# Optimization experiments

Measured on AMD Instinct MI355X. Metric: run time of the kernel, lower is better.

The kernel has to match this reference:

```python
import jax, jax.numpy as jnp
import numpy as np

N = 50000      # nodes
F_IN = 1024    # raw feature dim
D = 64         # student_dim = hidden_dim * compression_ratio
P = 3          # number of meta-paths
E = 1600000    # edges per meta-path adjacency (avg degree 32)


def setup_inputs() -> dict:
    key = jax.random.key(0)
    ks = jax.random.split(key, 10)
    feats = jax.random.normal(ks[0], (N, F_IN), jnp.float32)
    rows = jax.random.randint(ks[1], (P, E), 0, N, dtype=jnp.int32)
    cols = jax.random.randint(ks[2], (P, E), 0, N, dtype=jnp.int32)
    # normalized-adjacency-like positive edge weights
    vals = jax.random.uniform(ks[3], (P, E), jnp.float32) / 32.0
    # fc_list[0]: Linear(F_IN -> D), xavier_normal gain=1.414
    W0 = jax.random.normal(ks[4], (D, F_IN), jnp.float32) * 0.05
    b0 = jnp.zeros((D,), jnp.float32)
    # P GCN linear layers (D -> D, no bias) + GCN bias params
    Wg = jax.random.normal(ks[5], (P, D, D), jnp.float32) * 0.17
    bg = jnp.zeros((P, D), jnp.float32)
    # PReLU alpha (torch default init 0.25, one scalar per GCN)
    alpha = jnp.full((P,), 0.25, jnp.float32)
    # Attention: Linear(D -> D) and att vector [1, D]
    Wa = jax.random.normal(ks[6], (D, D), jnp.float32) * 0.17
    ba = jnp.zeros((D,), jnp.float32)
    att = jax.random.normal(ks[7], (1, D), jnp.float32) * 0.17
    return dict(feats=feats, rows=rows, cols=cols, vals=vals, W0=W0, b0=b0,
                Wg=Wg, bg=bg, alpha=alpha, Wa=Wa, ba=ba, att=att)


def reference(feats, rows, cols, vals, W0, b0, Wg, bg, alpha, Wa, ba, att):
    # h = elu(fc_list[0](feats))  (feat_drop = 0 -> identity)
    h = jax.nn.elu(feats @ W0.T + b0)                       # [N, D]
    embeds = []
    for i in range(P):
        s = h @ Wg[i].T                                     # [N, D]
        # sparse adj (COO) @ s : out[r] += v * s[c]
        msg = vals[i][:, None] * s[cols[i]]                 # [E, D]
        out = jax.ops.segment_sum(msg, rows[i], num_segments=N)
        out = out + bg[i]
        embeds.append(jnp.where(out > 0, out, alpha[i] * out))  # PReLU
    emb = jnp.stack(embeds)                                 # [P, N, D]
    # Attention over views: beta_i = att . mean_n tanh(fc(emb_i))
    sp = jnp.tanh(jnp.einsum('pnd,ed->pne', emb, Wa) + ba).mean(axis=1)  # [P, D]
    beta = jax.nn.softmax(sp @ att[0])                      # [P]
    z_mp = jnp.einsum('p,pnd->nd', beta, emb)               # [N, D]
    return z_mp
```

## Files before the change

kernel.cpp:

```cpp
#include <hip/hip_runtime.h>
#include <hip/hip_bf16.h>

#define N_NODES 50000
#define F_IN    1024
#define DD      64
#define PP      3
#define EE      1600000
#define NPC     98
#define CCAP    17664

typedef __attribute__((ext_vector_type(8))) short short8v;
typedef __attribute__((ext_vector_type(4))) float floatx4;
typedef __attribute__((ext_vector_type(2))) float floatx2;

__device__ inline float bfl(uint u) { return __uint_as_float(u << 16); }
__device__ inline float bfh(uint u) { return __uint_as_float(u & 0xffff0000u); }
__device__ inline floatx2 up2(uint u) {
    floatx2 r; r.x = bfl(u); r.y = bfh(u); return r;
}
__device__ inline uint cvtpk2(float a, float b) {
    __hip_bfloat162 h = __float22bfloat162_rn(make_float2(a, b));
    return *(uint*)&h;
}
__device__ inline ushort f2bf(float x) {
    __hip_bfloat16 h = __float2bfloat16(x);
    return *(ushort*)&h;
}

__global__ __launch_bounds__(256) void split_weights(const float* __restrict__ W0,
                                                     const float* __restrict__ Wg,
                                                     const float* __restrict__ Wa,
                                                     ushort* __restrict__ W0h,
                                                     ushort* __restrict__ Wgh,
                                                     ushort* __restrict__ Wah)
{
    int i = blockIdx.x * 256 + threadIdx.x;
    if (i < 64 * 1024) W0h[i] = f2bf(W0[i]);
    int j = i - 64 * 1024;
    if (j >= 0 && j < PP * 64 * 64) Wgh[j] = f2bf(Wg[j]);
    int k = i - 64 * 1024 - PP * 64 * 64;
    if (k >= 0 && k < 64 * 64) Wah[k] = f2bf(Wa[k]);
}

__global__ __launch_bounds__(256) void gemm1_partial(const float* __restrict__ feats,
                                                     const ushort* __restrict__ W0h,
                                                     float* __restrict__ hpart)
{
    __shared__ ushort Ah[64 * 64];
    __shared__ ushort Bh[64 * 64];
    const int t = threadIdx.x;
    const int w = t >> 6, lane = t & 63;
    const int row0 = blockIdx.x * 64;
    const int kh = blockIdx.y;
    const int l15 = lane & 15, l4 = lane >> 4;

    floatx4 acc[4] = {};
    float4 pa[4];
    uint4  pb[2];

    #pragma unroll
    for (int rep = 0; rep < 4; ++rep) {
        int idx = rep * 256 + t;
        int r = idx >> 4, c4 = idx & 15;
        int gr = row0 + r; if (gr >= N_NODES) gr = N_NODES - 1;
        pa[rep] = *(const float4*)&feats[(size_t)gr * F_IN + (kh * 8) * 64 + c4 * 4];
    }
    #pragma unroll
    for (int rep = 0; rep < 2; ++rep) {
        int idx = rep * 256 + t;
        int c = idx >> 3, u8 = idx & 7;
        pb[rep] = *(const uint4*)&W0h[(size_t)c * F_IN + (kh * 8) * 64 + u8 * 8];
    }

    for (int kc = 0; kc < 8; ++kc) {
        #pragma unroll
        for (int rep = 0; rep < 4; ++rep) {
            int idx = rep * 256 + t;
            int r = idx >> 4, c4 = idx & 15;
            int unit = (c4 >> 1) ^ (r & 7);
            int base = r * 64 + unit * 8 + (c4 & 1) * 4;
            *(uint2*)&Ah[base] = make_uint2(cvtpk2(pa[rep].x, pa[rep].y),
                                            cvtpk2(pa[rep].z, pa[rep].w));
        }
        #pragma unroll
        for (int rep = 0; rep < 2; ++rep) {
            int idx = rep * 256 + t;
            int c = idx >> 3, u8 = idx & 7;
            int unit = u8 ^ (c & 7);
            *(uint4*)&Bh[c * 64 + unit * 8] = pb[rep];
        }
        __syncthreads();

        if (kc < 7) {
            int g = kh * 8 + kc + 1;
            #pragma unroll
            for (int rep = 0; rep < 4; ++rep) {
                int idx = rep * 256 + t;
                int r = idx >> 4, c4 = idx & 15;
                int gr = row0 + r; if (gr >= N_NODES) gr = N_NODES - 1;
                pa[rep] = *(const float4*)&feats[(size_t)gr * F_IN + g * 64 + c4 * 4];
            }
            #pragma unroll
            for (int rep = 0; rep < 2; ++rep) {
                int idx = rep * 256 + t;
                int c = idx >> 3, u8 = idx & 7;
                pb[rep] = *(const uint4*)&W0h[(size_t)c * F_IN + g * 64 + u8 * 8];
            }
        }

        #pragma unroll
        for (int ks = 0; ks < 2; ++ks) {
            int arow = w * 16 + l15;
            int au = (ks * 4 + l4) ^ (arow & 7);
            short8v ah = *(short8v*)&Ah[arow * 64 + au * 8];
            #pragma unroll
            for (int cf = 0; cf < 4; ++cf) {
                int bcol = cf * 16 + l15;
                int bu = (ks * 4 + l4) ^ (bcol & 7);
                short8v bh = *(short8v*)&Bh[bcol * 64 + bu * 8];
                acc[cf] = __builtin_amdgcn_mfma_f32_16x16x32_bf16(ah, bh, acc[cf], 0, 0, 0);
            }
        }
        __syncthreads();
    }

    float* hp = hpart + ((size_t)(kh * 782 + blockIdx.x)) * 4096;
    #pragma unroll
    for (int cf = 0; cf < 4; ++cf)
        *(float4*)&hp[(cf * 256 + t) * 4] = make_float4(acc[cf][0], acc[cf][1],
                                                        acc[cf][2], acc[cf][3]);
}

__global__ __launch_bounds__(256) void gemm2_combine(const float* __restrict__ hpart,
                                                     const float* __restrict__ b0,
                                                     const ushort* __restrict__ Wgh,
                                                     ushort* __restrict__ s_all)
{
    __shared__ ushort Ah[64 * 64];
    __shared__ ushort Bh[64 * 64];
    __shared__ ushort Sout[64 * 64];
    const int t = threadIdx.x;
    const int w = t >> 6, lane = t & 63;
    const int row0 = blockIdx.x * 64;
    const int l15 = lane & 15, l4 = lane >> 4;

    const float* hp0 = hpart + (size_t)blockIdx.x * 4096;
    const float* hp1 = hpart + (size_t)(782 + blockIdx.x) * 4096;

    #pragma unroll
    for (int cf = 0; cf < 4; ++cf) {
        float4 a = *(const float4*)&hp0[(cf * 256 + t) * 4];
        float4 b = *(const float4*)&hp1[(cf * 256 + t) * 4];
        int col = cf * 16 + l15;
        float bias = b0[col];
        float xs[4] = {a.x + b.x + bias, a.y + b.y + bias,
                       a.z + b.z + bias, a.w + b.w + bias};
        #pragma unroll
        for (int r = 0; r < 4; ++r) {
            int row = w * 16 + l4 * 4 + r;
            float x = xs[r];
            x = x > 0.f ? x : (__expf(x) - 1.f);
            int u = (col >> 3) ^ (row & 7);
            Ah[row * 64 + u * 8 + (col & 7)] = f2bf(x);
        }
    }
    __syncthreads();

    for (int p = 0; p < PP; ++p) {
        #pragma unroll
        for (int rep = 0; rep < 2; ++rep) {
            int idx = rep * 256 + t;
            int r = idx >> 3, u8 = idx & 7;
            int unit = u8 ^ (r & 7);
            *(uint4*)&Bh[r * 64 + unit * 8] = *(const uint4*)&Wgh[(size_t)p * 4096 + idx * 8];
        }
        __syncthreads();

        floatx4 sacc[4] = {};
        #pragma unroll
        for (int ks = 0; ks < 2; ++ks) {
            int arow = w * 16 + l15;
            int au = (ks * 4 + l4) ^ (arow & 7);
            short8v ah = *(short8v*)&Ah[arow * 64 + au * 8];
            #pragma unroll
            for (int cf = 0; cf < 4; ++cf) {
                int bcol = cf * 16 + l15;
                int bu = (ks * 4 + l4) ^ (bcol & 7);
                short8v bh = *(short8v*)&Bh[bcol * 64 + bu * 8];
                sacc[cf] = __builtin_amdgcn_mfma_f32_16x16x32_bf16(ah, bh, sacc[cf], 0, 0, 0);
            }
        }
        #pragma unroll
        for (int cf = 0; cf < 4; ++cf) {
            int col = cf * 16 + l15;
            #pragma unroll
            for (int r = 0; r < 4; ++r)
                Sout[(w * 16 + l4 * 4 + r) * 64 + col] = f2bf(sacc[cf][r]);
        }
        __syncthreads();
        {
            int lr = t >> 2;
            int gr = row0 + lr;
            if (gr < N_NODES) {
                ushort* sp = s_all + (size_t)p * N_NODES * 64;
                int co = (t & 3) * 16;
                *(uint4*)&sp[(size_t)gr * 64 + co]     = *(uint4*)&Sout[lr * 64 + co];
                *(uint4*)&sp[(size_t)gr * 64 + co + 8] = *(uint4*)&Sout[lr * 64 + co + 8];
            }
        }
        __syncthreads();
    }
}

__global__ __launch_bounds__(256) void part1(const int*   __restrict__ rows,
                                             const int*   __restrict__ cols,
                                             const float* __restrict__ vals,
                                             int*   __restrict__ pcur3,
                                             uint2* __restrict__ coarsebuf)
{
    __shared__ uint2 stage[2560];
    __shared__ uint2 sorted[2560];
    __shared__ int cnt[128];
    __shared__ int sc[128];
    __shared__ int curb[128];
    __shared__ int gbase[128];
    const int t = threadIdx.x;
    const int path = blockIdx.y;
    const size_t ebase = (size_t)path * EE + (size_t)blockIdx.x * 2560;
    int* pcur = pcur3 + path * NPC;
    uint2* cb = coarsebuf + (size_t)path * NPC * CCAP;

    if (t < 128) { cnt[t] = 0; curb[t] = 0; }
    __syncthreads();

    #pragma unroll
    for (int it = 0; it < 10; ++it) {
        int e = it * 256 + t;
        int r = rows[ebase + e];
        int c = cols[ebase + e];
        float v = vals[ebase + e];
        int bin = r >> 9, rl = r & 511;
        stage[e] = make_uint2((uint)c | ((uint)rl << 16) | ((uint)bin << 25),
                              __float_as_uint(v));
        atomicAdd(&cnt[bin], 1);
    }
    __syncthreads();

    if (t < 128) sc[t] = cnt[t];
    __syncthreads();
    #pragma unroll
    for (int o = 1; o < 128; o <<= 1) {
        int v = (t < 128 && t >= o) ? sc[t - o] : 0;
        __syncthreads();
        if (t < 128 && t >= o) sc[t] += v;
        __syncthreads();
    }

    if (t < NPC) gbase[t] = atomicAdd(&pcur[t], cnt[t]);
    __syncthreads();

    #pragma unroll
    for (int it = 0; it < 10; ++it) {
        uint2 e = stage[it * 256 + t];
        int bin = e.x >> 25;
        int loc = (sc[bin] - cnt[bin]) + atomicAdd(&curb[bin], 1);
        sorted[loc] = e;
    }
    __syncthreads();

    #pragma unroll
    for (int it = 0; it < 10; ++it) {
        int i = it * 256 + t;
        uint2 e = sorted[i];
        int bin = e.x >> 25;
        int g = gbase[bin] + (i - (sc[bin] - cnt[bin]));
        if (g < CCAP) cb[(size_t)bin * CCAP + g] = e;
    }
}

__global__ __launch_bounds__(512) void sort2(const uint2* __restrict__ coarsebuf,
                                             const int*   __restrict__ pcur3,
                                             uint* __restrict__ sortpk,
                                             int* __restrict__ rowbeg3,
                                             int* __restrict__ rowend3)
{
    __shared__ int hist[512];
    __shared__ int cur[512];
    const int t = threadIdx.x;
    const int c = blockIdx.x, path = blockIdx.y;
    const int n = min(pcur3[path * NPC + c], CCAP);
    const size_t slabbase = ((size_t)path * NPC + c) * CCAP;
    const uint2* src = coarsebuf + slabbase;

    hist[t] = 0;
    __syncthreads();

    for (int i = t; i < n; i += 512)
        atomicAdd(&hist[(src[i].x >> 16) & 511], 1);
    __syncthreads();

    int c0 = hist[t];
    __syncthreads();
    #pragma unroll
    for (int o = 1; o < 512; o <<= 1) {
        int v = (t >= o) ? hist[t - o] : 0;
        __syncthreads();
        hist[t] += v;
        __syncthreads();
    }
    int excl = hist[t] - c0;
    cur[t] = excl;
    int gr = c * 512 + t;
    if (gr < N_NODES) {
        rowbeg3[path * N_NODES + gr] = (int)(slabbase + excl);
        rowend3[path * N_NODES + gr] = (int)(slabbase + excl + c0);
    }
    __syncthreads();

    for (int i = t; i < n; i += 512) {
        uint2 e = src[i];
        int rl = (e.x >> 16) & 511;
        int pos = atomicAdd(&cur[rl], 1);
        sortpk[slabbase + pos] = (e.x & 0xffffu) |
                                 ((uint)f2bf(__uint_as_float(e.y)) << 16);
    }
}

__global__ __launch_bounds__(256) void spmm_gather(const uint*   __restrict__ sortpk,
                                                   const int*    __restrict__ rowbeg3,
                                                   const int*    __restrict__ rowend3,
                                                   const ushort* __restrict__ s_all,
                                                   const float*  __restrict__ bg,
                                                   const float*  __restrict__ alpha,
                                                   ushort* __restrict__ emb)
{
    const int path = blockIdx.x / 12500;
    const int wid = (blockIdx.x % 12500) * 4 + (threadIdx.x >> 6);
    const int lane = threadIdx.x & 63;
    const int dq = lane & 7;
    const int slot = lane >> 3;
    const int e0 = rowbeg3[path * N_NODES + wid];
    const int e1 = rowend3[path * N_NODES + wid];
    const ushort* s_p = s_all + (size_t)path * N_NODES * 64;

    floatx2 acc[4] = {};
    if (e0 < e1) {
        const int last = e1 - 1;
        for (int e = e0; e < e1; e += 32) {
            int ea = e + slot, eb = ea + 8, ec = ea + 16, ed = ea + 24;
            uint pka = sortpk[min(ea, last)];
            uint pkb = sortpk[min(eb, last)];
            uint pkc = sortpk[min(ec, last)];
            uint pkd = sortpk[min(ed, last)];
            const uint4 ga = *(const uint4*)&s_p[(size_t)(pka & 0xffffu) * 64 + dq * 8];
            const uint4 gb = *(const uint4*)&s_p[(size_t)(pkb & 0xffffu) * 64 + dq * 8];
            const uint4 gc = *(const uint4*)&s_p[(size_t)(pkc & 0xffffu) * 64 + dq * 8];
            const uint4 gd = *(const uint4*)&s_p[(size_t)(pkd & 0xffffu) * 64 + dq * 8];
            float va = (ea <= last) ? bfh(pka) : 0.f;
            float vb = (eb <= last) ? bfh(pkb) : 0.f;
            float vc = (ec <= last) ? bfh(pkc) : 0.f;
            float vd = (ed <= last) ? bfh(pkd) : 0.f;
            floatx2 va2 = {va, va}, vb2 = {vb, vb}, vc2 = {vc, vc}, vd2 = {vd, vd};
            acc[0] += va2 * up2(ga.x); acc[1] += va2 * up2(ga.y);
            acc[2] += va2 * up2(ga.z); acc[3] += va2 * up2(ga.w);
            acc[0] += vb2 * up2(gb.x); acc[1] += vb2 * up2(gb.y);
            acc[2] += vb2 * up2(gb.z); acc[3] += vb2 * up2(gb.w);
            acc[0] += vc2 * up2(gc.x); acc[1] += vc2 * up2(gc.y);
            acc[2] += vc2 * up2(gc.z); acc[3] += vc2 * up2(gc.w);
            acc[0] += vd2 * up2(gd.x); acc[1] += vd2 * up2(gd.y);
            acc[2] += vd2 * up2(gd.z); acc[3] += vd2 * up2(gd.w);
        }
    }
    #pragma unroll
    for (int j = 0; j < 4; ++j) {
        acc[j].x += __shfl_xor(acc[j].x, 8);
        acc[j].y += __shfl_xor(acc[j].y, 8);
        acc[j].x += __shfl_xor(acc[j].x, 16);
        acc[j].y += __shfl_xor(acc[j].y, 16);
        acc[j].x += __shfl_xor(acc[j].x, 32);
        acc[j].y += __shfl_xor(acc[j].y, 32);
    }

    if (slot == 0) {
        const float al = alpha[path];
        const float* bgp = bg + path * 64;
        float x[8];
        #pragma unroll
        for (int j = 0; j < 4; ++j) {
            float v0 = acc[j].x + bgp[dq * 8 + 2 * j];
            float v1 = acc[j].y + bgp[dq * 8 + 2 * j + 1];
            x[2 * j]     = v0 > 0.f ? v0 : al * v0;
            x[2 * j + 1] = v1 > 0.f ? v1 : al * v1;
        }
        uint4 wv;
        wv.x = cvtpk2(x[0], x[1]);
        wv.y = cvtpk2(x[2], x[3]);
        wv.z = cvtpk2(x[4], x[5]);
        wv.w = cvtpk2(x[6], x[7]);
        *(uint4*)&emb[((size_t)path * N_NODES + wid) * 64 + dq * 8] = wv;
    }
}

__global__ __launch_bounds__(256) void postproc(const ushort* __restrict__ emb,
                                                const ushort* __restrict__ Wah,
                                                const float* __restrict__ ba,
                                                float* __restrict__ sp)
{
    __shared__ ushort Ah[64 * 64];
    __shared__ ushort Bh[64 * 64];
    __shared__ float red[16][64];
    const int t = threadIdx.x;
    const int w = t >> 6, lane = t & 63;
    const int l15 = lane & 15, l4 = lane >> 4;
    const int nb = (N_NODES + 63) >> 6;
    const int p  = blockIdx.x / nb;
    const int tb = blockIdx.x % nb;
    const int row0 = tb * 64;
    const ushort* embp = emb + (size_t)p * N_NODES * 64;

    #pragma unroll
    for (int rep = 0; rep < 2; ++rep) {
        int idx = rep * 256 + t;
        int r = idx >> 3, u8 = idx & 7;
        int gr = row0 + r; if (gr >= N_NODES) gr = N_NODES - 1;
        int unit = u8 ^ (r & 7);
        *(uint4*)&Ah[r * 64 + unit * 8] = *(const uint4*)&embp[(size_t)gr * 64 + u8 * 8];
        *(uint4*)&Bh[r * 64 + unit * 8] = *(const uint4*)&Wah[idx * 8];
    }
    __syncthreads();

    floatx4 acc[4] = {};
    #pragma unroll
    for (int ks = 0; ks < 2; ++ks) {
        int arow = w * 16 + l15;
        int au = (ks * 4 + l4) ^ (arow & 7);
        short8v ah = *(short8v*)&Ah[arow * 64 + au * 8];
        #pragma unroll
        for (int cf = 0; cf < 4; ++cf) {
            int bcol = cf * 16 + l15;
            int bu = (ks * 4 + l4) ^ (bcol & 7);
            short8v bh = *(short8v*)&Bh[bcol * 64 + bu * 8];
            acc[cf] = __builtin_amdgcn_mfma_f32_16x16x32_bf16(ah, bh, acc[cf], 0, 0, 0);
        }
    }

    #pragma unroll
    for (int cf = 0; cf < 4; ++cf) {
        int col = cf * 16 + l15;
        float s = 0.f;
        #pragma unroll
        for (int r = 0; r < 4; ++r) {
            int gr = row0 + w * 16 + l4 * 4 + r;
            if (gr < N_NODES) s += tanhf(acc[cf][r] + ba[col]);
        }
        red[w * 4 + l4][col] = s;
    }
    __syncthreads();
    if (t < 64) {
        float ssum = 0.f;
        #pragma unroll
        for (int g = 0; g < 16; ++g) ssum += red[g][t];
        unsafeAtomicAdd(&sp[p * 64 + t], ssum);
    }
}

__global__ void beta_kernel(const float* __restrict__ sp,
                            const float* __restrict__ att,
                            float* __restrict__ beta)
{
    int lane = threadIdx.x;
    float w[PP];
    #pragma unroll
    for (int p = 0; p < PP; ++p) {
        float x = sp[p * 64 + lane] * (1.0f / (float)N_NODES) * att[lane];
        #pragma unroll
        for (int off = 32; off; off >>= 1) x += __shfl_down(x, off);
        w[p] = __shfl(x, 0);
    }
    if (lane == 0) {
        float mx = fmaxf(w[0], fmaxf(w[1], w[2]));
        float e0 = __expf(w[0] - mx);
        float e1 = __expf(w[1] - mx);
        float e2 = __expf(w[2] - mx);
        float s = e0 + e1 + e2;
        beta[0] = e0 / s; beta[1] = e1 / s; beta[2] = e2 / s;
    }
}

__global__ __launch_bounds__(256) void combine(const ushort* __restrict__ emb,
                                               const float* __restrict__ beta,
                                               float* __restrict__ out)
{
    const float b0 = beta[0], b1 = beta[1], b2 = beta[2];
    const size_t tot = (size_t)N_NODES * 64;
    size_t i = ((size_t)blockIdx.x * 256 + threadIdx.x) * 8;
    if (i < tot) {
        uint4 e0 = *(const uint4*)&emb[i];
        uint4 e1 = *(const uint4*)&emb[tot + i];
        uint4 e2 = *(const uint4*)&emb[2 * tot + i];
        float o[8];
        o[0] = b0*bfl(e0.x) + b1*bfl(e1.x) + b2*bfl(e2.x);
        o[1] = b0*bfh(e0.x) + b1*bfh(e1.x) + b2*bfh(e2.x);
        o[2] = b0*bfl(e0.y) + b1*bfl(e1.y) + b2*bfl(e2.y);
        o[3] = b0*bfh(e0.y) + b1*bfh(e1.y) + b2*bfh(e2.y);
        o[4] = b0*bfl(e0.z) + b1*bfl(e1.z) + b2*bfl(e2.z);
        o[5] = b0*bfh(e0.z) + b1*bfh(e1.z) + b2*bfh(e2.z);
        o[6] = b0*bfl(e0.w) + b1*bfl(e1.w) + b2*bfl(e2.w);
        o[7] = b0*bfh(e0.w) + b1*bfh(e1.w) + b2*bfh(e2.w);
        *(float4*)&out[i]     = make_float4(o[0], o[1], o[2], o[3]);
        *(float4*)&out[i + 4] = make_float4(o[4], o[5], o[6], o[7]);
    }
}

extern "C" void kernel_launch(void* const* d_in, const int* in_sizes, int n_in,
                              void* d_out, int out_size, void* d_ws, size_t ws_size,
                              hipStream_t stream)
{
    const float* feats = (const float*)d_in[0];
    const int*   rows  = (const int*)  d_in[1];
    const int*   cols  = (const int*)  d_in[2];
    const float* vals  = (const float*)d_in[3];
    const float* W0    = (const float*)d_in[4];
    const float* b0    = (const float*)d_in[5];
    const float* Wg    = (const float*)d_in[6];
    const float* bg    = (const float*)d_in[7];
    const float* alpha = (const float*)d_in[8];
    const float* Wa    = (const float*)d_in[9];
    const float* ba    = (const float*)d_in[10];
    const float* att   = (const float*)d_in[11];
    float* out = (float*)d_out;

    const size_t ND = (size_t)N_NODES * 64;
    char* base = (char*)d_ws;
    ushort* emb    = (ushort*)base;              base += 3 * ND * 2;
    ushort* s_all  = (ushort*)base;              base += 3 * ND * 2;
    ushort* W0h    = (ushort*)base;              base += 64 * 1024 * 2;
    ushort* Wgh    = (ushort*)base;              base += PP * 64 * 64 * 2;
    ushort* Wah    = (ushort*)base;              base += 64 * 64 * 2;
    int*    pcur3  = (int*)base;                 base += PP * NPC * 4;
    float*  sp     = (float*)base;               base += 192 * 4;
    float*  beta   = (float*)base;               base += 64 * 4;
    int*    rowbeg3 = (int*)base;                base += PP * N_NODES * 4;
    int*    rowend3 = (int*)base;                base += PP * N_NODES * 4;
    base = (char*)(((size_t)base + 255) & ~(size_t)255);
    float*  hpart  = (float*)base;               base += (size_t)2 * 782 * 4096 * 4;
    uint2*  coarsebuf = (uint2*)base;            base += (size_t)PP * NPC * CCAP * 8;
    uint*   sortpk    = (uint*)base;             base += (size_t)PP * NPC * CCAP * 4;

    hipMemsetAsync(pcur3, 0, (PP * NPC + 192) * sizeof(int), stream);

    split_weights<<<(64 * 1024 + PP * 64 * 64 + 64 * 64 + 255) / 256, 256, 0, stream>>>(
        W0, Wg, Wa, W0h, Wgh, Wah);

    gemm1_partial<<<dim3(782, 2), 256, 0, stream>>>(feats, W0h, hpart);
    gemm2_combine<<<782, 256, 0, stream>>>(hpart, b0, Wgh, s_all);

    part1<<<dim3(EE / 2560, 3), 256, 0, stream>>>(rows, cols, vals, pcur3, coarsebuf);
    sort2<<<dim3(NPC, 3), 512, 0, stream>>>(coarsebuf, pcur3, sortpk, rowbeg3, rowend3);
    spmm_gather<<<3 * 12500, 256, 0, stream>>>(
        sortpk, rowbeg3, rowend3, s_all, bg, alpha, emb);

    postproc<<<3 * 782, 256, 0, stream>>>(emb, Wah, ba, sp);
    beta_kernel<<<1, 64, 0, stream>>>(sp, att, beta);
    combine<<<(int)((ND / 8 + 255) / 256), 256, 0, stream>>>(emb, beta, out);
}
```

Measured before the change: 319.4 us.

## Stage full W0 half-slice in LDS and stream feats directly into MFMA registers

gemm1_partial now uses 512-thread blocks covering 128 rows. Each block loads its whole 64x512 bf16 slice of W0 into LDS once. Each lane then reads its feats A-fragments straight from global memory, converts them to bf16 in registers and feeds the MFMA, so A no longer goes through LDS and the per-chunk barriers are gone. This is meant to remove the LDS staging and sync overhead of the memory-bound first GEMM. The trade-off is 64KB of LDS per block, which limits occupancy, and direct global loads of feats with no explicit prefetch. gemm2_combine's indexing into hpart is updated to match the new partial layout.

```diff
diff --git a/kernel.cpp b/kernel.cpp
--- a/kernel.cpp
+++ b/kernel.cpp
@@ -8,6 +8,7 @@
 #define EE      1600000
 #define NPC     98
 #define CCAP    17664
+#define NB1     391
 
 typedef __attribute__((ext_vector_type(8))) short short8v;
 typedef __attribute__((ext_vector_type(4))) float floatx4;
@@ -42,92 +43,52 @@
     if (k >= 0 && k < 64 * 64) Wah[k] = f2bf(Wa[k]);
 }
 
-__global__ __launch_bounds__(256) void gemm1_partial(const float* __restrict__ feats,
+__global__ __launch_bounds__(512) void gemm1_partial(const float* __restrict__ feats,
                                                      const ushort* __restrict__ W0h,
                                                      float* __restrict__ hpart)
 {
-    __shared__ ushort Ah[64 * 64];
-    __shared__ ushort Bh[64 * 64];
+    __shared__ ushort Bh[64 * 512];
     const int t = threadIdx.x;
     const int w = t >> 6, lane = t & 63;
-    const int row0 = blockIdx.x * 64;
+    const int row0 = blockIdx.x * 128;
     const int kh = blockIdx.y;
     const int l15 = lane & 15, l4 = lane >> 4;
 
+    #pragma unroll
+    for (int rep = 0; rep < 8; ++rep) {
+        int id = rep * 512 + t;
+        int d = id >> 6, uu = id & 63;
+        *(uint4*)&Bh[d * 512 + ((uu ^ (d & 7)) << 3)] =
+            *(const uint4*)&W0h[(size_t)d * F_IN + kh * 512 + uu * 8];
+    }
+    __syncthreads();
+
+    int gr = row0 + w * 16 + l15;
+    if (gr >= N_NODES) gr = N_NODES - 1;
+    const float* arow = feats + (size_t)gr * F_IN + kh * 512 + l4 * 8;
+
     floatx4 acc[4] = {};
-    float4 pa[4];
-    uint4  pb[2];
-
-    #pragma unroll
-    for (int rep = 0; rep < 4; ++rep) {
-        int idx = rep * 256 + t;
-        int r = idx >> 4, c4 = idx & 15;
-        int gr = row0 + r; if (gr >= N_NODES) gr = N_NODES - 1;
-        pa[rep] = *(const float4*)&feats[(size_t)gr * F_IN + (kh * 8) * 64 + c4 * 4];
-    }
-    #pragma unroll
-    for (int rep = 0; rep < 2; ++rep) {
-        int idx = rep * 256 + t;
-        int c = idx >> 3, u8 = idx & 7;
-        pb[rep] = *(const uint4*)&W0h[(size_t)c * F_IN + (kh * 8) * 64 + u8 * 8];
-    }
-
-    for (int kc = 0; kc < 8; ++kc) {
-        #pragma unroll
-        for (int rep = 0; rep < 4; ++rep) {
-            int idx = rep * 256 + t;
-            int r = idx >> 4, c4 = idx & 15;
-            int unit = (c4 >> 1) ^ (r & 7);
-            int base = r * 64 + unit * 8 + (c4 & 1) * 4;
-            *(uint2*)&Ah[base] = make_uint2(cvtpk2(pa[rep].x, pa[rep].y),
-                                            cvtpk2(pa[rep].z, pa[rep].w));
-        }
-        #pragma unroll
-        for (int rep = 0; rep < 2; ++rep) {
-            int idx = rep * 256 + t;
-            int c = idx >> 3, u8 = idx & 7;
-            int unit = u8 ^ (c & 7);
-            *(uint4*)&Bh[c * 64 + unit * 8] = pb[rep];
-        }
-        __syncthreads();
-
-        if (kc < 7) {
-            int g = kh * 8 + kc + 1;
-            #pragma unroll
-            for (int rep = 0; rep < 4; ++rep) {
-                int idx = rep * 256 + t;
-                int r = idx >> 4, c4 = idx & 15;
-                int gr = row0 + r; if (gr >= N_NODES) gr = N_NODES - 1;
-                pa[rep] = *(const float4*)&feats[(size_t)gr * F_IN + g * 64 + c4 * 4];
-            }
-            #pragma unroll
-            for (int rep = 0; rep < 2; ++rep) {
-                int idx = rep * 256 + t;
-                int c = idx >> 3, u8 = idx & 7;
-                pb[rep] = *(const uint4*)&W0h[(size_t)c * F_IN + g * 64 + u8 * 8];
-            }
-        }
-
-        #pragma unroll
-        for (int ks = 0; ks < 2; ++ks) {
-            int arow = w * 16 + l15;
-            int au = (ks * 4 + l4) ^ (arow & 7);
-            short8v ah = *(short8v*)&Ah[arow * 64 + au * 8];
-            #pragma unroll
-            for (int cf = 0; cf < 4; ++cf) {
-                int bcol = cf * 16 + l15;
-                int bu = (ks * 4 + l4) ^ (bcol & 7);
-                short8v bh = *(short8v*)&Bh[bcol * 64 + bu * 8];
-                acc[cf] = __builtin_amdgcn_mfma_f32_16x16x32_bf16(ah, bh, acc[cf], 0, 0, 0);
-            }
-        }
-        __syncthreads();
-    }
-
-    float* hp = hpart + ((size_t)(kh * 782 + blockIdx.x)) * 4096;
+    #pragma unroll 4
+    for (int ks = 0; ks < 16; ++ks) {
+        float4 a0 = *(const float4*)&arow[ks * 32];
+        float4 a1 = *(const float4*)&arow[ks * 32 + 4];
+        uint4 av;
+        av.x = cvtpk2(a0.x, a0.y); av.y = cvtpk2(a0.z, a0.w);
+        av.z = cvtpk2(a1.x, a1.y); av.w = cvtpk2(a1.z, a1.w);
+        short8v ah = *(short8v*)&av;
+        int u = ks * 4 + l4;
+        #pragma unroll
+        for (int cf = 0; cf < 4; ++cf) {
+            int d = cf * 16 + l15;
+            short8v bh = *(short8v*)&Bh[d * 512 + ((u ^ (d & 7)) << 3)];
+            acc[cf] = __builtin_amdgcn_mfma_f32_16x16x32_bf16(ah, bh, acc[cf], 0, 0, 0);
+        }
+    }
+
+    float* hp = hpart + ((size_t)(kh * NB1 + blockIdx.x)) * 8192;
     #pragma unroll
     for (int cf = 0; cf < 4; ++cf)
-        *(float4*)&hp[(cf * 256 + t) * 4] = make_float4(acc[cf][0], acc[cf][1],
+        *(float4*)&hp[(cf * 512 + t) * 4] = make_float4(acc[cf][0], acc[cf][1],
                                                         acc[cf][2], acc[cf][3]);
 }
 
@@ -142,15 +103,17 @@
     const int t = threadIdx.x;
     const int w = t >> 6, lane = t & 63;
     const int row0 = blockIdx.x * 64;
+    const int bi = blockIdx.x >> 1;
+    const int hh = blockIdx.x & 1;
     const int l15 = lane & 15, l4 = lane >> 4;
 
-    const float* hp0 = hpart + (size_t)blockIdx.x * 4096;
-    const float* hp1 = hpart + (size_t)(782 + blockIdx.x) * 4096;
+    const float* hp0 = hpart + (size_t)bi * 8192;
+    const float* hp1 = hpart + (size_t)(NB1 + bi) * 8192;
 
     #pragma unroll
     for (int cf = 0; cf < 4; ++cf) {
-        float4 a = *(const float4*)&hp0[(cf * 256 + t) * 4];
-        float4 b = *(const float4*)&hp1[(cf * 256 + t) * 4];
+        float4 a = *(const float4*)&hp0[(cf * 512 + hh * 256 + t) * 4];
+        float4 b = *(const float4*)&hp1[(cf * 512 + hh * 256 + t) * 4];
         int col = cf * 16 + l15;
         float bias = b0[col];
         float xs[4] = {a.x + b.x + bias, a.y + b.y + bias,
@@ -179,9 +142,9 @@
         floatx4 sacc[4] = {};
         #pragma unroll
         for (int ks = 0; ks < 2; ++ks) {
-            int arow = w * 16 + l15;
-            int au = (ks * 4 + l4) ^ (arow & 7);
-            short8v ah = *(short8v*)&Ah[arow * 64 + au * 8];
+            int arow2 = w * 16 + l15;
+            int au = (ks * 4 + l4) ^ (arow2 & 7);
+            short8v ah = *(short8v*)&Ah[arow2 * 64 + au * 8];
             #pragma unroll
             for (int cf = 0; cf < 4; ++cf) {
                 int bcol = cf * 16 + l15;
@@ -543,7 +506,7 @@
     int*    rowbeg3 = (int*)base;                base += PP * N_NODES * 4;
     int*    rowend3 = (int*)base;                base += PP * N_NODES * 4;
     base = (char*)(((size_t)base + 255) & ~(size_t)255);
-    float*  hpart  = (float*)base;               base += (size_t)2 * 782 * 4096 * 4;
+    float*  hpart  = (float*)base;               base += (size_t)2 * NB1 * 8192 * 4;
     uint2*  coarsebuf = (uint2*)base;            base += (size_t)PP * NPC * CCAP * 8;
     uint*   sortpk    = (uint*)base;             base += (size_t)PP * NPC * CCAP * 4;
 
@@ -552,7 +515,7 @@
     split_weights<<<(64 * 1024 + PP * 64 * 64 + 64 * 64 + 255) / 256, 256, 0, stream>>>(
         W0, Wg, Wa, W0h, Wgh, Wah);
 
-    gemm1_partial<<<dim3(782, 2), 256, 0, stream>>>(feats, W0h, hpart);
+    gemm1_partial<<<dim3(NB1, 2), 512, 0, stream>>>(feats, W0h, hpart);
     gemm2_combine<<<782, 256, 0, stream>>>(hpart, b0, Wgh, s_all);
 
     part1<<<dim3(EE / 2560, 3), 256, 0, stream>>>(rows, cols, vals, pcur3, coarsebuf);
```

New measurement: 306.2 us. 1.04x faster.
